# Kernel tuning notes

Measured on AMD Instinct MI355X. Metric: run time of the kernel, lower is better.

The kernel has to match this reference:

```python
import jax, jax.numpy as jnp
import numpy as np

N_NODES = 50000
N_EDGES = 500000
IN_FEATS = 64
HIDDEN = 64
OUT_FEATS = 8
N_LAYERS = 6
NEG_SLOPE = 0.2
LN_EPS = 1e-5


def setup_inputs() -> dict:
    key = jax.random.key(0)
    ks = jax.random.split(key, 12)
    s_in = 1.0 / np.sqrt(IN_FEATS)
    s_h = 1.0 / np.sqrt(HIDDEN)
    return {
        "nodes": jax.random.normal(ks[0], (N_NODES, IN_FEATS), jnp.float32),
        "src": jax.random.randint(ks[1], (N_EDGES,), 0, N_NODES, jnp.int32),
        "dst": jax.random.randint(ks[2], (N_EDGES,), 0, N_NODES, jnp.int32),
        "w_in": jax.random.normal(ks[3], (IN_FEATS, HIDDEN), jnp.float32) * s_in,
        "b_in": jnp.zeros((HIDDEN,), jnp.float32),
        "w_src": jax.random.normal(ks[4], (N_LAYERS, HIDDEN, HIDDEN), jnp.float32) * s_h,
        "b_src": jnp.zeros((N_LAYERS, HIDDEN), jnp.float32),
        "w_dst": jax.random.normal(ks[5], (N_LAYERS, HIDDEN, HIDDEN), jnp.float32) * s_h,
        "b_dst": jnp.zeros((N_LAYERS, HIDDEN), jnp.float32),
        "attn": jax.random.normal(ks[6], (N_LAYERS, HIDDEN), jnp.float32) * s_h,
        "gamma": jnp.ones((N_LAYERS, HIDDEN), jnp.float32),
        "beta": jnp.zeros((N_LAYERS, HIDDEN), jnp.float32),
        "w_out": jax.random.normal(ks[7], (HIDDEN, OUT_FEATS), jnp.float32) * s_h,
        "b_out": jnp.zeros((OUT_FEATS,), jnp.float32),
    }


def _layernorm(x, g, b):
    m = jnp.mean(x, axis=-1, keepdims=True)
    v = jnp.mean(jnp.square(x - m), axis=-1, keepdims=True)
    return (x - m) * jax.lax.rsqrt(v + LN_EPS) * g + b


def _gatv2(h, src, dst, ws, bs, wd, bd, a, n_nodes):
    # GATv2Conv, num_heads=1 (DGL semantics)
    fs = h @ ws + bs                                  # [N, H] fc_src
    fd = h @ wd + bd                                  # [N, H] fc_dst
    e = jax.nn.leaky_relu(fs[src] + fd[dst], NEG_SLOPE)  # [E, H]
    score = e @ a                                     # [E]
    # segment softmax over incoming edges of each dst node
    mx = jax.ops.segment_max(score, dst, num_segments=n_nodes)
    ex = jnp.exp(score - mx[dst])
    denom = jax.ops.segment_sum(ex, dst, num_segments=n_nodes)
    alpha = ex / denom[dst]                           # [E]
    return jax.ops.segment_sum(alpha[:, None] * fs[src], dst, num_segments=n_nodes)


def reference(nodes, src, dst, w_in, b_in, w_src, b_src, w_dst, b_dst, attn, gamma, beta, w_out, b_out):
    n = nodes.shape[0]
    h = nodes @ w_in + b_in
    for i in range(N_LAYERS):
        t = _gatv2(h, src, dst, w_src[i], b_src[i], w_dst[i], b_dst[i], attn[i], n)
        t = _layernorm(t, gamma[i], beta[i])
        h = h + jax.nn.gelu(t, approximate=False)
    return h @ w_out + b_out
```

## Files before the change

### kernel.cpp

```cpp
#include <hip/hip_runtime.h>
#include <math.h>

#define N_NODES 50000
#define N_EDGES 500000
#define NLAYERS 6
#define NEG_SLOPE 0.2f
#define LN_EPS 1e-5f
#define SCAN_B 1024
#define NSCAN_BLOCKS ((N_NODES + SCAN_B - 1) / SCAN_B)
#define LOG2E 1.4426950408889634f

typedef __attribute__((ext_vector_type(8))) short short8;
typedef __attribute__((ext_vector_type(4))) float f32x4;

__device__ __forceinline__ float wave_sum64(float v) {
#pragma unroll
    for (int m = 32; m >= 1; m >>= 1) v += __shfl_xor(v, m, 64);
    return v;
}

__device__ __forceinline__ int wave_incl_scan(int v, int lane) {
#pragma unroll
    for (int offs = 1; offs < 64; offs <<= 1) {
        int t = __shfl_up(v, offs, 64);
        if (lane >= offs) v += t;
    }
    return v;
}

__device__ __forceinline__ unsigned bf16_rne(float v) {
    unsigned u = __float_as_uint(v);
    return (u + 0x7fffu + ((u >> 16) & 1u)) >> 16;
}

__device__ __forceinline__ float fast_exp2(float x) {
    float r;
    asm("v_exp_f32 %0, %1" : "=v"(r) : "v"(x));
    return r;
}

__device__ __forceinline__ float4 bf4_to_f4(ushort4 u) {
    float4 r;
    r.x = __uint_as_float((unsigned)u.x << 16);
    r.y = __uint_as_float((unsigned)u.y << 16);
    r.z = __uint_as_float((unsigned)u.z << 16);
    r.w = __uint_as_float((unsigned)u.w << 16);
    return r;
}

__global__ void count_deg(const int* __restrict__ dst, int* __restrict__ deg,
                          int* __restrict__ hist) {
    if (blockIdx.x == 0 && threadIdx.x < 64) hist[threadIdx.x] = 0;
    int i = blockIdx.x * blockDim.x + threadIdx.x;
    if (i < N_EDGES) atomicAdd(&deg[dst[i]], 1);
}

__global__ void scan1(const int* __restrict__ deg, int* __restrict__ row_ptr,
                      int* __restrict__ bsum, int* __restrict__ hist) {
    __shared__ int lhist[64];
    __shared__ int wtot[16];
    int t = threadIdx.x;
    if (t < 64) lhist[t] = 0;
    int i = blockIdx.x * SCAN_B + t;
    int lane = t & 63, wv = t >> 6;
    int v = (i < N_NODES) ? deg[i] : 0;
    __syncthreads();
    if (i < N_NODES) atomicAdd(&lhist[min(v, 63)], 1);
    int incl = wave_incl_scan(v, lane);
    if (lane == 63) wtot[wv] = incl;
    __syncthreads();
    if (wv == 0) {
        int wval = (lane < 16) ? wtot[lane] : 0;
        int ws = wave_incl_scan(wval, lane);
        if (lane < 16) wtot[lane] = ws - wval;
    }
    __syncthreads();
    int excl = incl - v + wtot[wv];
    if (i < N_NODES) row_ptr[i] = excl;
    if (t == SCAN_B - 1) bsum[blockIdx.x] = excl + v;
    if (t < 64) atomicAdd(&hist[t], lhist[t]);
}

__global__ void scan3(int* __restrict__ row_ptr, const int* __restrict__ bsum,
                      int* __restrict__ pos, const int* __restrict__ hist,
                      int* __restrict__ binpos) {
    __shared__ int boff_s;
    int t = threadIdx.x;
    if (t < 64) {
        int v = (t < NSCAN_BLOCKS && t < (int)blockIdx.x) ? bsum[t] : 0;
#pragma unroll
        for (int m = 32; m >= 1; m >>= 1) v += __shfl_xor(v, m, 64);
        if (t == 0) boff_s = v;
    }
    if (blockIdx.x == 0 && t >= 64 && t < 128) {
        int lane = t - 64;
        int v = hist[lane];
        int incl = wave_incl_scan(v, lane);
        binpos[lane] = incl - v;
    }
    __syncthreads();
    int i = blockIdx.x * SCAN_B + t;
    if (i < N_NODES) {
        int r = row_ptr[i] + boff_s;
        row_ptr[i] = r;
        pos[i] = r;
    }
    if (i == 0) row_ptr[N_NODES] = N_EDGES;
}

__global__ void bucket_nodes(const int* __restrict__ deg, int* __restrict__ binpos,
                             int* __restrict__ perm) {
    __shared__ int lhist[64], lbase[64];
    int t = threadIdx.x;
    if (t < 64) lhist[t] = 0;
    __syncthreads();
    int i = blockIdx.x * SCAN_B + t;
    int b = 0;
    if (i < N_NODES) {
        b = min(deg[i], 63);
        atomicAdd(&lhist[b], 1);
    }
    __syncthreads();
    if (t < 64) {
        lbase[t] = atomicAdd(&binpos[t], lhist[t]);
        lhist[t] = 0;
    }
    __syncthreads();
    if (i < N_NODES) {
        int r = atomicAdd(&lhist[b], 1);
        perm[lbase[b] + r] = i;
    }
}

__global__ void scatter_edges(const int* __restrict__ dst, const int* __restrict__ src,
                              int* __restrict__ pos, int* __restrict__ srcs) {
    int i = blockIdx.x * blockDim.x + threadIdx.x;
    if (i < N_EDGES) {
        int p = atomicAdd(&pos[dst[i]], 1);
        srcs[p] = src[i];
    }
}

__global__ void pack_w(const float* __restrict__ w_in, const float* __restrict__ w_src,
                       const float* __restrict__ w_dst, unsigned short* __restrict__ wpk_hi,
                       unsigned short* __restrict__ wpk_lo) {
    int b = blockIdx.x;
    const float* W = (b == 0) ? w_in
                              : (b <= 6 ? w_src + (size_t)(b - 1) * 4096
                                        : w_dst + (size_t)(b - 7) * 4096);
    unsigned short* hi = wpk_hi + (size_t)b * 4096;
    unsigned short* lo = wpk_lo + (size_t)b * 4096;
    for (int idx = threadIdx.x; idx < 4096; idx += 256) {
        int t = idx >> 10;
        int s = (idx >> 9) & 1;
        int l = (idx >> 3) & 63;
        int j = idx & 7;
        int row = s * 32 + (l >> 4) * 8 + j;
        int col = t * 16 + (l & 15);
        float v = W[row * 64 + col];
        unsigned rh = bf16_rne(v);
        float hf = __uint_as_float(rh << 16);
        unsigned rl = bf16_rne(v - hf);
        hi[idx] = (unsigned short)rh;
        lo[idx] = (unsigned short)rl;
    }
}

__device__ __forceinline__ void load_split8(const float* __restrict__ p, short8& hi, short8& lo) {
    float4 x0 = *(const float4*)p;
    float4 x1 = *(const float4*)(p + 4);
    float v[8] = {x0.x, x0.y, x0.z, x0.w, x1.x, x1.y, x1.z, x1.w};
#pragma unroll
    for (int j = 0; j < 8; ++j) {
        unsigned rh = bf16_rne(v[j]);
        float hf = __uint_as_float(rh << 16);
        unsigned rl = bf16_rne(v[j] - hf);
        hi[j] = (short)rh;
        lo[j] = (short)rl;
    }
}

__device__ __forceinline__ void mfma_16rows(const short8 ah0, const short8 ah1, const short8 al0,
                                            const short8 al1,
                                            const unsigned short* __restrict__ whi,
                                            const unsigned short* __restrict__ wlo, int lane,
                                            f32x4 acc[4]) {
#pragma unroll
    for (int t = 0; t < 4; ++t) {
#pragma unroll
        for (int s = 0; s < 2; ++s) {
            const size_t boff = ((size_t)((t * 2 + s) * 64 + lane)) * 8;
            short8 bh = *(const short8*)(whi + boff);
            short8 bl = *(const short8*)(wlo + boff);
            short8 a_h = s ? ah1 : ah0;
            short8 a_l = s ? al1 : al0;
            acc[t] = __builtin_amdgcn_mfma_f32_16x16x32_bf16(a_h, bh, acc[t], 0, 0, 0);
            acc[t] = __builtin_amdgcn_mfma_f32_16x16x32_bf16(a_l, bh, acc[t], 0, 0, 0);
            acc[t] = __builtin_amdgcn_mfma_f32_16x16x32_bf16(a_h, bl, acc[t], 0, 0, 0);
        }
    }
}

__global__ void mfma_in_proj(const float* __restrict__ X, const unsigned short* __restrict__ whi,
                             const unsigned short* __restrict__ wlo,
                             const float* __restrict__ bias, float* __restrict__ H) {
    int lane = threadIdx.x & 63, wv = threadIdx.x >> 6;
    int R = blockIdx.x * 64 + wv * 16;
    int arow = min(R + (lane & 15), N_NODES - 1);
    const float* p = X + (size_t)arow * 64 + (lane >> 4) * 8;
    short8 ah0, ah1, al0, al1;
    load_split8(p, ah0, al0);
    load_split8(p + 32, ah1, al1);
    f32x4 acc[4];
    f32x4 z = {0.f, 0.f, 0.f, 0.f};
#pragma unroll
    for (int t = 0; t < 4; ++t) acc[t] = z;
    mfma_16rows(ah0, ah1, al0, al1, whi, wlo, lane, acc);
    int crow = R + (lane >> 4) * 4;
#pragma unroll
    for (int t = 0; t < 4; ++t) {
        int col = t * 16 + (lane & 15);
        float bv = bias[col];
#pragma unroll
        for (int r = 0; r < 4; ++r) {
            int row = crow + r;
            if (row < N_NODES) H[(size_t)row * 64 + col] = acc[t][r] + bv;
        }
    }
}

__global__ void mfma_dual(const float* __restrict__ X, const unsigned short* __restrict__ wshi,
                          const unsigned short* __restrict__ wslo, const float* __restrict__ bs,
                          const unsigned short* __restrict__ wdhi,
                          const unsigned short* __restrict__ wdlo, const float* __restrict__ bd,
                          unsigned short* __restrict__ FS, float* __restrict__ FD) {
    int lane = threadIdx.x & 63, wv = threadIdx.x >> 6;
    int R = blockIdx.x * 64 + wv * 16;
    int arow = min(R + (lane & 15), N_NODES - 1);
    const float* p = X + (size_t)arow * 64 + (lane >> 4) * 8;
    short8 ah0, ah1, al0, al1;
    load_split8(p, ah0, al0);
    load_split8(p + 32, ah1, al1);
    f32x4 accS[4], accD[4];
    f32x4 z = {0.f, 0.f, 0.f, 0.f};
#pragma unroll
    for (int t = 0; t < 4; ++t) {
        accS[t] = z;
        accD[t] = z;
    }
    mfma_16rows(ah0, ah1, al0, al1, wshi, wslo, lane, accS);
    mfma_16rows(ah0, ah1, al0, al1, wdhi, wdlo, lane, accD);
    int crow = R + (lane >> 4) * 4;
#pragma unroll
    for (int t = 0; t < 4; ++t) {
        int col = t * 16 + (lane & 15);
        float bsv = bs[col], bdv = bd[col];
#pragma unroll
        for (int r = 0; r < 4; ++r) {
            int row = crow + r;
            if (row < N_NODES) {
                FS[(size_t)row * 64 + col] = (unsigned short)bf16_rne(accS[t][r] + bsv);
                FD[(size_t)row * 64 + col] = accD[t][r] + bdv;
            }
        }
    }
}

#define WPB 4
__global__ void node_fused_kernel(const unsigned short* __restrict__ fs,
                                  const float* __restrict__ fd, const int* __restrict__ row_ptr,
                                  const int* __restrict__ srcs, const int* __restrict__ perm,
                                  const float* __restrict__ attn, const float* __restrict__ gamma,
                                  const float* __restrict__ beta, float* __restrict__ h) {
    __shared__ float xpose[WPB][64];
    int lane = threadIdx.x & 63;
    int wv = threadIdx.x >> 6;
    int q = lane >> 4;
    int ql = lane & 15;
    int f0 = ql << 2;
    int idx = blockIdx.x * WPB + wv;
    if (idx >= N_NODES) return;
    int n = perm[idx];
    float gL = gamma[lane], bL = beta[lane];
    float hval = h[(size_t)n * 64 + lane];
    float4 a4 = *(const float4*)&attn[f0];
    a4.x *= LOG2E;
    a4.y *= LOG2E;
    a4.z *= LOG2E;
    a4.w *= LOG2E;
    int beg = row_ptr[n], end = row_ptr[n + 1];
    int deg = end - beg;
    float4 fd4 = *(const float4*)&fd[(size_t)n * 64 + f0];
    float d = 0.f;
    float4 acc = make_float4(0.f, 0.f, 0.f, 0.f);
    for (int c0 = 0; c0 < deg; c0 += 64) {
        int cl = min(64, deg - c0);
        int sv = (lane < cl) ? srcs[beg + c0 + lane] : 0;
        int nt = (cl + 3) >> 2;
        ushort4 rowA = make_ushort4(0, 0, 0, 0), rowB = rowA;
        int sid0 = __shfl(sv, q, 64);
        if (q < cl) rowA = *(const ushort4*)&fs[(size_t)sid0 * 64 + f0];
        int sid1 = __shfl(sv, (4 + q) & 63, 64);
        if (4 + q < cl) rowB = *(const ushort4*)&fs[(size_t)sid1 * 64 + f0];
        for (int t = 0; t < nt; ++t) {
            int eoff = 4 * t + q;
            bool valid = eoff < cl;
            float4 cur = bf4_to_f4(rowA);
            rowA = rowB;
            int e2 = 4 * (t + 2) + q;
            int sid2 = __shfl(sv, e2 & 63, 64);
            if (e2 < cl) rowB = *(const ushort4*)&fs[(size_t)sid2 * 64 + f0];
            float vx = cur.x + fd4.x, vy = cur.y + fd4.y;
            float vz = cur.z + fd4.z, vw = cur.w + fd4.w;
            vx = fmaxf(vx, NEG_SLOPE * vx);
            vy = fmaxf(vy, NEG_SLOPE * vy);
            vz = fmaxf(vz, NEG_SLOPE * vz);
            vw = fmaxf(vw, NEG_SLOPE * vw);
            float sp = fmaf(a4.x, vx, fmaf(a4.y, vy, fmaf(a4.z, vz, a4.w * vw)));
            sp += __shfl_xor(sp, 1, 64);
            sp += __shfl_xor(sp, 2, 64);
            sp += __shfl_xor(sp, 4, 64);
            sp += __shfl_xor(sp, 8, 64);
            float w = valid ? fast_exp2(sp) : 0.f;
            d += w;
            acc.x = fmaf(w, cur.x, acc.x);
            acc.y = fmaf(w, cur.y, acc.y);
            acc.z = fmaf(w, cur.z, acc.z);
            acc.w = fmaf(w, cur.w, acc.w);
        }
    }
    d += __shfl_xor(d, 16, 64);
    d += __shfl_xor(d, 32, 64);
    acc.x += __shfl_xor(acc.x, 16, 64);
    acc.y += __shfl_xor(acc.y, 16, 64);
    acc.z += __shfl_xor(acc.z, 16, 64);
    acc.w += __shfl_xor(acc.w, 16, 64);
    acc.x += __shfl_xor(acc.x, 32, 64);
    acc.y += __shfl_xor(acc.y, 32, 64);
    acc.z += __shfl_xor(acc.z, 32, 64);
    acc.w += __shfl_xor(acc.w, 32, 64);
    float inv = (d > 0.f) ? 1.f / d : 0.f;
    acc.x *= inv;
    acc.y *= inv;
    acc.z *= inv;
    acc.w *= inv;
    if (q == 0) *(float4*)&xpose[wv][f0] = acc;
    float val = xpose[wv][lane];
    float mean = wave_sum64(val) * 0.015625f;
    float dev = val - mean;
    float var = wave_sum64(dev * dev) * 0.015625f;
    float rstd = rsqrtf(var + LN_EPS);
    float tval = fmaf(dev * rstd, gL, bL);
    float g = 0.5f * tval * (1.f + erff(tval * 0.70710678118654752f));
    h[(size_t)n * 64 + lane] = hval + g;
}

__global__ void out_proj_kernel(const float* __restrict__ h, const float* __restrict__ W,
                                const float* __restrict__ b, float* __restrict__ out) {
    __shared__ float Ws[64 * 8];
    __shared__ float bs[8];
    __shared__ float Hs[32][65];
    int t = threadIdx.x;
    for (int i = t; i < 512; i += 256) Ws[i] = W[i];
    if (t < 8) bs[t] = b[t];
    int n0 = blockIdx.x * 32;
    for (int i = t; i < 32 * 64; i += 256) {
        int r = i >> 6, c = i & 63;
        int n = n0 + r;
        Hs[r][c] = (n < N_NODES) ? h[(size_t)n * 64 + c] : 0.f;
    }
    __syncthreads();
    int nl = t >> 3, o = t & 7;
    int n = n0 + nl;
    if (n >= N_NODES) return;
    float acc = bs[o];
#pragma unroll
    for (int k = 0; k < 64; ++k) acc = fmaf(Hs[nl][k], Ws[k * 8 + o], acc);
    out[(size_t)n * 8 + o] = acc;
}

extern "C" void kernel_launch(void* const* d_in, const int* in_sizes, int n_in,
                              void* d_out, int out_size, void* d_ws, size_t ws_size,
                              hipStream_t stream) {
    const float* nodes = (const float*)d_in[0];
    const int* src = (const int*)d_in[1];
    const int* dst = (const int*)d_in[2];
    const float* w_in = (const float*)d_in[3];
    const float* b_in = (const float*)d_in[4];
    const float* w_src = (const float*)d_in[5];
    const float* b_src = (const float*)d_in[6];
    const float* w_dst = (const float*)d_in[7];
    const float* b_dst = (const float*)d_in[8];
    const float* attn = (const float*)d_in[9];
    const float* gamma = (const float*)d_in[10];
    const float* beta = (const float*)d_in[11];
    const float* w_out = (const float*)d_in[12];
    const float* b_out = (const float*)d_in[13];
    float* out = (float*)d_out;

    char* ws = (char*)d_ws;
    size_t off = 0;
    auto alloc = [&](size_t bytes) {
        void* p = ws + off;
        off += (bytes + 255) & ~(size_t)255;
        return p;
    };
    float* h = (float*)alloc((size_t)N_NODES * 64 * 4);
    unsigned short* fs = (unsigned short*)alloc((size_t)N_NODES * 64 * 2);
    float* fd = (float*)alloc((size_t)N_NODES * 64 * 4);
    unsigned short* wpk_hi = (unsigned short*)alloc((size_t)13 * 4096 * 2);
    unsigned short* wpk_lo = (unsigned short*)alloc((size_t)13 * 4096 * 2);
    int* deg = (int*)alloc((size_t)N_NODES * 4);
    int* row_ptr = (int*)alloc((size_t)(N_NODES + 1) * 4);
    int* pos = (int*)alloc((size_t)N_NODES * 4);
    int* srcs = (int*)alloc((size_t)N_EDGES * 4);
    int* bsum = (int*)alloc((size_t)NSCAN_BLOCKS * 4);
    int* hist = (int*)alloc((size_t)64 * 4);
    int* binpos = (int*)alloc((size_t)64 * 4);
    int* perm = (int*)alloc((size_t)N_NODES * 4);

    hipMemsetAsync(deg, 0, (size_t)N_NODES * 4, stream);
    count_deg<<<(N_EDGES + 255) / 256, 256, 0, stream>>>(dst, deg, hist);
    scan1<<<NSCAN_BLOCKS, SCAN_B, 0, stream>>>(deg, row_ptr, bsum, hist);
    scan3<<<NSCAN_BLOCKS, SCAN_B, 0, stream>>>(row_ptr, bsum, pos, hist, binpos);
    bucket_nodes<<<NSCAN_BLOCKS, SCAN_B, 0, stream>>>(deg, binpos, perm);
    scatter_edges<<<(N_EDGES + 255) / 256, 256, 0, stream>>>(dst, src, pos, srcs);

    pack_w<<<13, 256, 0, stream>>>(w_in, w_src, w_dst, wpk_hi, wpk_lo);

    mfma_in_proj<<<(N_NODES + 63) / 64, 256, 0, stream>>>(nodes, wpk_hi, wpk_lo, b_in, h);

    for (int l = 0; l < NLAYERS; ++l) {
        mfma_dual<<<(N_NODES + 63) / 64, 256, 0, stream>>>(
            h, wpk_hi + (size_t)(1 + l) * 4096, wpk_lo + (size_t)(1 + l) * 4096,
            b_src + (size_t)l * 64, wpk_hi + (size_t)(7 + l) * 4096,
            wpk_lo + (size_t)(7 + l) * 4096, b_dst + (size_t)l * 64, fs, fd);
        node_fused_kernel<<<(N_NODES + WPB - 1) / WPB, 256, 0, stream>>>(
            fs, fd, row_ptr, srcs, perm, attn + (size_t)l * 64, gamma + (size_t)l * 64,
            beta + (size_t)l * 64, h);
    }

    out_proj_kernel<<<(N_NODES + 31) / 32, 256, 0, stream>>>(h, w_out, b_out, out);
}
```

Before: 347.6 us.

## Renumber nodes into degree-sorted order so all per-node arrays are permuted

Instead of indexing nodes through a degree-sorted perm array inside the per-layer aggregation kernel, the graph is relabelled once. CSR row pointers and source indices are built in permuted node order, input rows are gathered through perm, and outputs are scattered back through perm at the end. This makes h, fs and fd accesses in the fused node kernel contiguous per block and removes the perm indirection from every layer. The cost is extra preprocessing kernels and an inverse-permutation array, and neighbour gather locality now depends on the new numbering.

```diff
diff --git a/kernel.cpp b/kernel.cpp
--- a/kernel.cpp
+++ b/kernel.cpp
@@ -55,61 +55,26 @@
     if (i < N_EDGES) atomicAdd(&deg[dst[i]], 1);
 }
 
-__global__ void scan1(const int* __restrict__ deg, int* __restrict__ row_ptr,
-                      int* __restrict__ bsum, int* __restrict__ hist) {
+__global__ void histo(const int* __restrict__ deg, int* __restrict__ hist) {
     __shared__ int lhist[64];
-    __shared__ int wtot[16];
     int t = threadIdx.x;
     if (t < 64) lhist[t] = 0;
+    __syncthreads();
     int i = blockIdx.x * SCAN_B + t;
-    int lane = t & 63, wv = t >> 6;
-    int v = (i < N_NODES) ? deg[i] : 0;
-    __syncthreads();
-    if (i < N_NODES) atomicAdd(&lhist[min(v, 63)], 1);
+    if (i < N_NODES) atomicAdd(&lhist[min(deg[i], 63)], 1);
+    __syncthreads();
+    if (t < 64) atomicAdd(&hist[t], lhist[t]);
+}
+
+__global__ void binscan(const int* __restrict__ hist, int* __restrict__ binpos) {
+    int lane = threadIdx.x;
+    int v = hist[lane];
     int incl = wave_incl_scan(v, lane);
-    if (lane == 63) wtot[wv] = incl;
-    __syncthreads();
-    if (wv == 0) {
-        int wval = (lane < 16) ? wtot[lane] : 0;
-        int ws = wave_incl_scan(wval, lane);
-        if (lane < 16) wtot[lane] = ws - wval;
-    }
-    __syncthreads();
-    int excl = incl - v + wtot[wv];
-    if (i < N_NODES) row_ptr[i] = excl;
-    if (t == SCAN_B - 1) bsum[blockIdx.x] = excl + v;
-    if (t < 64) atomicAdd(&hist[t], lhist[t]);
-}
-
-__global__ void scan3(int* __restrict__ row_ptr, const int* __restrict__ bsum,
-                      int* __restrict__ pos, const int* __restrict__ hist,
-                      int* __restrict__ binpos) {
-    __shared__ int boff_s;
-    int t = threadIdx.x;
-    if (t < 64) {
-        int v = (t < NSCAN_BLOCKS && t < (int)blockIdx.x) ? bsum[t] : 0;
-#pragma unroll
-        for (int m = 32; m >= 1; m >>= 1) v += __shfl_xor(v, m, 64);
-        if (t == 0) boff_s = v;
-    }
-    if (blockIdx.x == 0 && t >= 64 && t < 128) {
-        int lane = t - 64;
-        int v = hist[lane];
-        int incl = wave_incl_scan(v, lane);
-        binpos[lane] = incl - v;
-    }
-    __syncthreads();
-    int i = blockIdx.x * SCAN_B + t;
-    if (i < N_NODES) {
-        int r = row_ptr[i] + boff_s;
-        row_ptr[i] = r;
-        pos[i] = r;
-    }
-    if (i == 0) row_ptr[N_NODES] = N_EDGES;
+    binpos[lane] = incl - v;
 }
 
 __global__ void bucket_nodes(const int* __restrict__ deg, int* __restrict__ binpos,
-                             int* __restrict__ perm) {
+                             int* __restrict__ perm, int* __restrict__ inv_perm) {
     __shared__ int lhist[64], lbase[64];
     int t = threadIdx.x;
     if (t < 64) lhist[t] = 0;
@@ -128,16 +93,61 @@
     __syncthreads();
     if (i < N_NODES) {
         int r = atomicAdd(&lhist[b], 1);
-        perm[lbase[b] + r] = i;
-    }
+        int p = lbase[b] + r;
+        perm[p] = i;
+        inv_perm[i] = p;
+    }
+}
+
+__global__ void scan1p(const int* __restrict__ deg, const int* __restrict__ perm,
+                       int* __restrict__ row_ptr_p, int* __restrict__ bsum) {
+    __shared__ int wtot[16];
+    int t = threadIdx.x;
+    int i = blockIdx.x * SCAN_B + t;
+    int lane = t & 63, wv = t >> 6;
+    int v = (i < N_NODES) ? deg[perm[i]] : 0;
+    int incl = wave_incl_scan(v, lane);
+    if (lane == 63) wtot[wv] = incl;
+    __syncthreads();
+    if (wv == 0) {
+        int wval = (lane < 16) ? wtot[lane] : 0;
+        int ws = wave_incl_scan(wval, lane);
+        if (lane < 16) wtot[lane] = ws - wval;
+    }
+    __syncthreads();
+    int excl = incl - v + wtot[wv];
+    if (i < N_NODES) row_ptr_p[i] = excl;
+    if (t == SCAN_B - 1) bsum[blockIdx.x] = excl + v;
+}
+
+__global__ void scan3p(int* __restrict__ row_ptr_p, const int* __restrict__ bsum,
+                       int* __restrict__ pos_p) {
+    __shared__ int boff_s;
+    int t = threadIdx.x;
+    if (t < 64) {
+        int v = (t < NSCAN_BLOCKS && t < (int)blockIdx.x) ? bsum[t] : 0;
+#pragma unroll
+        for (int m = 32; m >= 1; m >>= 1) v += __shfl_xor(v, m, 64);
+        if (t == 0) boff_s = v;
+    }
+    __syncthreads();
+    int i = blockIdx.x * SCAN_B + t;
+    if (i < N_NODES) {
+        int r = row_ptr_p[i] + boff_s;
+        row_ptr_p[i] = r;
+        pos_p[i] = r;
+    }
+    if (i == 0) row_ptr_p[N_NODES] = N_EDGES;
 }
 
 __global__ void scatter_edges(const int* __restrict__ dst, const int* __restrict__ src,
-                              int* __restrict__ pos, int* __restrict__ srcs) {
+                              const int* __restrict__ inv_perm, int* __restrict__ pos_p,
+                              int* __restrict__ srcs_p) {
     int i = blockIdx.x * blockDim.x + threadIdx.x;
     if (i < N_EDGES) {
-        int p = atomicAdd(&pos[dst[i]], 1);
-        srcs[p] = src[i];
+        int dp = inv_perm[dst[i]];
+        int p = atomicAdd(&pos_p[dp], 1);
+        srcs_p[p] = inv_perm[src[i]];
     }
 }
 
@@ -201,12 +211,13 @@
     }
 }
 
-__global__ void mfma_in_proj(const float* __restrict__ X, const unsigned short* __restrict__ whi,
+__global__ void mfma_in_proj(const float* __restrict__ X, const int* __restrict__ perm,
+                             const unsigned short* __restrict__ whi,
                              const unsigned short* __restrict__ wlo,
                              const float* __restrict__ bias, float* __restrict__ H) {
     int lane = threadIdx.x & 63, wv = threadIdx.x >> 6;
     int R = blockIdx.x * 64 + wv * 16;
-    int arow = min(R + (lane & 15), N_NODES - 1);
+    int arow = perm[min(R + (lane & 15), N_NODES - 1)];
     const float* p = X + (size_t)arow * 64 + (lane >> 4) * 8;
     short8 ah0, ah1, al0, al1;
     load_split8(p, ah0, al0);
@@ -269,18 +280,17 @@
 #define WPB 4
 __global__ void node_fused_kernel(const unsigned short* __restrict__ fs,
                                   const float* __restrict__ fd, const int* __restrict__ row_ptr,
-                                  const int* __restrict__ srcs, const int* __restrict__ perm,
-                                  const float* __restrict__ attn, const float* __restrict__ gamma,
-                                  const float* __restrict__ beta, float* __restrict__ h) {
+                                  const int* __restrict__ srcs, const float* __restrict__ attn,
+                                  const float* __restrict__ gamma, const float* __restrict__ beta,
+                                  float* __restrict__ h) {
     __shared__ float xpose[WPB][64];
     int lane = threadIdx.x & 63;
     int wv = threadIdx.x >> 6;
     int q = lane >> 4;
     int ql = lane & 15;
     int f0 = ql << 2;
-    int idx = blockIdx.x * WPB + wv;
-    if (idx >= N_NODES) return;
-    int n = perm[idx];
+    int n = blockIdx.x * WPB + wv;
+    if (n >= N_NODES) return;
     float gL = gamma[lane], bL = beta[lane];
     float hval = h[(size_t)n * 64 + lane];
     float4 a4 = *(const float4*)&attn[f0];
@@ -355,8 +365,9 @@
     h[(size_t)n * 64 + lane] = hval + g;
 }
 
-__global__ void out_proj_kernel(const float* __restrict__ h, const float* __restrict__ W,
-                                const float* __restrict__ b, float* __restrict__ out) {
+__global__ void out_proj_kernel(const float* __restrict__ h, const int* __restrict__ perm,
+                                const float* __restrict__ W, const float* __restrict__ b,
+                                float* __restrict__ out) {
     __shared__ float Ws[64 * 8];
     __shared__ float bs[8];
     __shared__ float Hs[32][65];
@@ -376,7 +387,7 @@
     float acc = bs[o];
 #pragma unroll
     for (int k = 0; k < 64; ++k) acc = fmaf(Hs[nl][k], Ws[k * 8 + o], acc);
-    out[(size_t)n * 8 + o] = acc;
+    out[(size_t)perm[n] * 8 + o] = acc;
 }
 
 extern "C" void kernel_launch(void* const* d_in, const int* in_sizes, int n_in,
@@ -411,24 +422,27 @@
     unsigned short* wpk_hi = (unsigned short*)alloc((size_t)13 * 4096 * 2);
     unsigned short* wpk_lo = (unsigned short*)alloc((size_t)13 * 4096 * 2);
     int* deg = (int*)alloc((size_t)N_NODES * 4);
-    int* row_ptr = (int*)alloc((size_t)(N_NODES + 1) * 4);
-    int* pos = (int*)alloc((size_t)N_NODES * 4);
-    int* srcs = (int*)alloc((size_t)N_EDGES * 4);
+    int* row_ptr_p = (int*)alloc((size_t)(N_NODES + 1) * 4);
+    int* pos_p = (int*)alloc((size_t)N_NODES * 4);
+    int* srcs_p = (int*)alloc((size_t)N_EDGES * 4);
     int* bsum = (int*)alloc((size_t)NSCAN_BLOCKS * 4);
     int* hist = (int*)alloc((size_t)64 * 4);
     int* binpos = (int*)alloc((size_t)64 * 4);
     int* perm = (int*)alloc((size_t)N_NODES * 4);
+    int* inv_perm = (int*)alloc((size_t)N_NODES * 4);
 
     hipMemsetAsync(deg, 0, (size_t)N_NODES * 4, stream);
     count_deg<<<(N_EDGES + 255) / 256, 256, 0, stream>>>(dst, deg, hist);
-    scan1<<<NSCAN_BLOCKS, SCAN_B, 0, stream>>>(deg, row_ptr, bsum, hist);
-    scan3<<<NSCAN_BLOCKS, SCAN_B, 0, stream>>>(row_ptr, bsum, pos, hist, binpos);
-    bucket_nodes<<<NSCAN_BLOCKS, SCAN_B, 0, stream>>>(deg, binpos, perm);
-    scatter_edges<<<(N_EDGES + 255) / 256, 256, 0, stream>>>(dst, src, pos, srcs);
+    histo<<<NSCAN_BLOCKS, SCAN_B, 0, stream>>>(deg, hist);
+    binscan<<<1, 64, 0, stream>>>(hist, binpos);
+    bucket_nodes<<<NSCAN_BLOCKS, SCAN_B, 0, stream>>>(deg, binpos, perm, inv_perm);
+    scan1p<<<NSCAN_BLOCKS, SCAN_B, 0, stream>>>(deg, perm, row_ptr_p, bsum);
+    scan3p<<<NSCAN_BLOCKS, SCAN_B, 0, stream>>>(row_ptr_p, bsum, pos_p);
+    scatter_edges<<<(N_EDGES + 255) / 256, 256, 0, stream>>>(dst, src, inv_perm, pos_p, srcs_p);
 
     pack_w<<<13, 256, 0, stream>>>(w_in, w_src, w_dst, wpk_hi, wpk_lo);
 
-    mfma_in_proj<<<(N_NODES + 63) / 64, 256, 0, stream>>>(nodes, wpk_hi, wpk_lo, b_in, h);
+    mfma_in_proj<<<(N_NODES + 63) / 64, 256, 0, stream>>>(nodes, perm, wpk_hi, wpk_lo, b_in, h);
 
     for (int l = 0; l < NLAYERS; ++l) {
         mfma_dual<<<(N_NODES + 63) / 64, 256, 0, stream>>>(
@@ -436,9 +450,9 @@
             b_src + (size_t)l * 64, wpk_hi + (size_t)(7 + l) * 4096,
             wpk_lo + (size_t)(7 + l) * 4096, b_dst + (size_t)l * 64, fs, fd);
         node_fused_kernel<<<(N_NODES + WPB - 1) / WPB, 256, 0, stream>>>(
-            fs, fd, row_ptr, srcs, perm, attn + (size_t)l * 64, gamma + (size_t)l * 64,
+            fs, fd, row_ptr_p, srcs_p, attn + (size_t)l * 64, gamma + (size_t)l * 64,
             beta + (size_t)l * 64, h);
     }
 
-    out_proj_kernel<<<(N_NODES + 31) / 32, 256, 0, stream>>>(h, w_out, b_out, out);
-}
+    out_proj_kernel<<<(N_NODES + 31) / 32, 256, 0, stream>>>(h, perm, w_out, b_out, out);
+}
```

Measured after the change: 346.7 us. Within noise of the previous version (-0.3%).
